# Optimization experiments

Measured on AMD Instinct MI355X. Metric: run time of the kernel, lower is better.

## Reference

```python
import jax, jax.numpy as jnp
import numpy as np

BN_EPS = 1e-5  # torch BatchNorm1d default


def _batchnorm(x, gamma, beta):
    # x: [B, N, H]. torch BatchNorm1d on 3D input normalizes per channel (dim 1 = N)
    # over batch and last dim, using biased variance (training mode).
    mean = jnp.mean(x, axis=(0, 2), keepdims=True)
    var = jnp.var(x, axis=(0, 2), keepdims=True)
    return gamma[None, :, None] * (x - mean) / jnp.sqrt(var + BN_EPS) + beta[None, :, None]


def setup_inputs() -> dict:
    key = jax.random.key(0)
    ks = jax.random.split(key, 8)
    B, N, D, Hd = 4, 256, 128, 256
    # symmetric Bernoulli(0.05) adjacency, zero diagonal
    raw = (jax.random.uniform(ks[0], (B, N, N)) < 0.05).astype(jnp.float32)
    A = jnp.maximum(raw, jnp.swapaxes(raw, 1, 2))
    A = A * (1.0 - jnp.eye(N, dtype=jnp.float32))
    X = jax.random.normal(ks[1], (B, N, D), dtype=jnp.float32)

    def lin(k, fi, fo):
        return (jax.random.normal(k, (fi, fo), dtype=jnp.float32) / np.sqrt(fi).astype(np.float32))

    W1 = lin(ks[2], D, Hd); b1 = jnp.zeros((Hd,), jnp.float32)
    g1 = jnp.ones((N,), jnp.float32); be1 = jnp.zeros((N,), jnp.float32)
    W2 = lin(ks[3], Hd, Hd); b2 = jnp.zeros((Hd,), jnp.float32)
    g2 = jnp.ones((N,), jnp.float32); be2 = jnp.zeros((N,), jnp.float32)
    W3 = lin(ks[4], D, Hd); b3 = jnp.zeros((Hd,), jnp.float32)
    W4 = lin(ks[5], Hd, D); b4 = jnp.zeros((D,), jnp.float32)
    eps = jnp.full((1,), 0.1, dtype=jnp.float32)  # reset_parameters: 0.1/sqrt(1)
    return dict(A=A, X=X, eps=eps, W1=W1, b1=b1, g1=g1, be1=be1,
                W2=W2, b2=b2, g2=g2, be2=be2, W3=W3, b3=b3, W4=W4, b4=b4)


def reference(A, X, eps, W1, b1, g1, be1, W2, b2, g2, be2, W3, b3, W4, b4):
    B, N, D = X.shape
    I = jnp.eye(N, dtype=A.dtype)
    # standard GIN-style propagation: ((1+eps)*I + A) @ X
    X_std = ((1.0 + eps[0]) * I[None, :, :] + A) @ X

    # triangle/pair aggregation. Original: for node i, for each neighbor pair
    # (j<k) with A[j,k] != 0, add mlp2(X[j]+X[k]).
    # Vectorized: X_pw[b,i] = sum_{j<k} A[b,i,j]*A[b,i,k]*A[b,j,k]*mlp2(X[b,j]+X[b,k])
    P = X[:, :, None, :] + X[:, None, :, :]                       # [B,N,N,D] pair sums
    Fp = jax.nn.relu(jax.nn.relu(P @ W3 + b3) @ W4 + b4)          # mlp2 (dropout p=0)
    triu = jnp.triu(jnp.ones((N, N), A.dtype), k=1)               # j<k only
    G = (A * triu)[..., None] * Fp                                # [B,N,N,D]
    X_pw = jnp.einsum('bij,bik,bjkd->bid', A, A, G)

    Xn = X_std + X_pw
    # mlp1: Linear -> Dropout(0) -> ReLU -> BN -> Linear -> Dropout(0) -> ReLU -> BN
    h = _batchnorm(jax.nn.relu(Xn @ W1 + b1), g1, be1)
    h = _batchnorm(jax.nn.relu(h @ W2 + b2), g2, be2)
    return h
```

## Files before the change

kernel.cpp:

```cpp
#include <hip/hip_runtime.h>
#include <hip/hip_bf16.h>
#include <stdint.h>

#define B 4
#define N 256
#define D 128
#define H 256
#define MAXE 4096
#define SLOTCAP 256

typedef __attribute__((ext_vector_type(8))) short bf16x8;
typedef __attribute__((ext_vector_type(4))) float f32x4;

__device__ __forceinline__ ushort f2b(float f) {
  __hip_bfloat16 h = __float2bfloat16(f);
  return *reinterpret_cast<ushort*>(&h);
}
__device__ __forceinline__ float b2f(ushort u) {
  return __uint_as_float(((unsigned)u) << 16);
}

#define SWZ(off, row) ((off) ^ (((row) & 7) << 4))

__global__ __launch_bounds__(64) void k_adj(
    const float* __restrict__ A, const float* __restrict__ W3,
    const float* __restrict__ W4,
    uint64_t* __restrict__ adjMask, unsigned* __restrict__ deg,
    uint8_t* __restrict__ nbr, unsigned* __restrict__ rowBase,
    unsigned* __restrict__ edgeCnt, unsigned* __restrict__ edges,
    ushort* __restrict__ W3T, ushort* __restrict__ W4T) {
  int bid = blockIdx.x, lane = threadIdx.x;
  if (bid >= B * N) {
    int idx = (bid - B * N) * 64 + lane;
    if (idx < D * H) {
      int h = idx >> 7, c = idx & 127;
      W3T[h * D + c] = f2b(W3[c * H + h]);
    } else {
      int i2 = idx - D * H;
      int d = i2 >> 8, hh = i2 & 255;
      W4T[d * H + hh] = f2b(W4[hh * D + d]);
    }
    return;
  }
  int row = bid;
  int b = row >> 8, j = row & 255;
  const float* Arow = A + (size_t)row * N;
  uint64_t m0 = __ballot(Arow[lane] != 0.0f);
  uint64_t m1 = __ballot(Arow[64 + lane] != 0.0f);
  uint64_t m2 = __ballot(Arow[128 + lane] != 0.0f);
  uint64_t m3 = __ballot(Arow[192 + lane] != 0.0f);
  if (lane == 0) {
    adjMask[row * 4 + 0] = m0; adjMask[row * 4 + 1] = m1;
    adjMask[row * 4 + 2] = m2; adjMask[row * 4 + 3] = m3;
  }
  int c0 = __popcll(m0), c1 = __popcll(m1), c2 = __popcll(m2), c3 = __popcll(m3);
  int total = min(c0 + c1 + c2 + c3, 64);
  if (lane == 0) deg[row] = (unsigned)total;
  uint64_t lt = (1ull << lane) - 1ull;
  uint8_t* nr = nbr + (size_t)row * 64;
  if ((m0 >> lane) & 1) { int s = __popcll(m0 & lt);              if (s < 64) nr[s] = (uint8_t)lane; }
  if ((m1 >> lane) & 1) { int s = c0 + __popcll(m1 & lt);         if (s < 64) nr[s] = (uint8_t)(64+lane); }
  if ((m2 >> lane) & 1) { int s = c0+c1 + __popcll(m2 & lt);      if (s < 64) nr[s] = (uint8_t)(128+lane); }
  if ((m3 >> lane) & 1) { int s = c0+c1+c2 + __popcll(m3 & lt);   if (s < 64) nr[s] = (uint8_t)(192+lane); }
  auto gtm = [&](int c) -> uint64_t {
    int lo = j - c * 64;
    if (lo < 0) return ~0ull;
    if (lo >= 63) return 0ull;
    return ~((2ull << lo) - 1ull);
  };
  uint64_t e0 = m0 & gtm(0), e1 = m1 & gtm(1), e2 = m2 & gtm(2), e3 = m3 & gtm(3);
  int t0c = __popcll(e0), t1c = __popcll(e1), t2c = __popcll(e2);
  int et = t0c + t1c + t2c + __popcll(e3);
  unsigned base = 0;
  if (lane == 0 && et) base = atomicAdd(&edgeCnt[b], (unsigned)et);
  base = (unsigned)__shfl((int)base, 0);
  if (lane == 0) rowBase[row] = base;
  unsigned* eb = edges + (size_t)b * MAXE;
  unsigned tag = ((unsigned)j << 8);
  if ((e0 >> lane) & 1) { unsigned s = base + __popcll(e0 & lt);               if (s < MAXE) eb[s] = tag | (unsigned)lane; }
  if ((e1 >> lane) & 1) { unsigned s = base + t0c + __popcll(e1 & lt);         if (s < MAXE) eb[s] = tag | (unsigned)(64+lane); }
  if ((e2 >> lane) & 1) { unsigned s = base + t0c+t1c + __popcll(e2 & lt);     if (s < MAXE) eb[s] = tag | (unsigned)(128+lane); }
  if ((e3 >> lane) & 1) { unsigned s = base + t0c+t1c+t2c + __popcll(e3 & lt); if (s < MAXE) eb[s] = tag | (unsigned)(192+lane); }
}

__global__ __launch_bounds__(256) void k_edge_mlp(
    const float* __restrict__ X, const unsigned* __restrict__ edges,
    const unsigned* __restrict__ edgeCnt,
    const ushort* __restrict__ W3T, const float* __restrict__ b3,
    const ushort* __restrict__ W4T, const float* __restrict__ b4,
    ushort* __restrict__ Fp) {
  __shared__ __align__(16) char smem[12288];
  __shared__ unsigned eLds[16];
  int blk = blockIdx.x;
  int b = blk >> 8, tile = blk & 255;
  unsigned cnt = min(edgeCnt[b], (unsigned)MAXE);
  int t0 = tile * 16;
  if ((unsigned)t0 >= cnt) return;
  int nE = min(16, (int)(cnt - (unsigned)t0));
  int tid = threadIdx.x;
  int w = tid >> 6, l = tid & 63, r = l & 15, g = l >> 4;
  const float* Xb = X + ((size_t)b * N) * D;

  if (tid < 16) eLds[tid] = (tid < nE) ? edges[(size_t)b * MAXE + t0 + tid] : 0u;
  __syncthreads();
  for (int idx = tid; idx < 16 * 64; idx += 256) {
    int e = idx >> 6, cp = idx & 63;
    unsigned ev = eLds[e];
    int j = (int)((ev >> 8) & 255u), k = (int)(ev & 255u);
    float2 xa = *(const float2*)(Xb + (size_t)j * D + cp * 2);
    float2 xb = *(const float2*)(Xb + (size_t)k * D + cp * 2);
    unsigned pk = (unsigned)f2b(xa.x + xb.x) | ((unsigned)f2b(xa.y + xb.y) << 16);
    *(unsigned*)(smem + e * 256 + SWZ(cp * 4, e)) = pk;
  }
  __syncthreads();
  {
    bf16x8 afr[4];
#pragma unroll
    for (int ks = 0; ks < 4; ++ks)
      afr[ks] = *(const bf16x8*)(smem + r * 256 + SWZ(ks * 64 + g * 16, r));
    f32x4 acc[4];
#pragma unroll
    for (int t4 = 0; t4 < 4; ++t4) acc[t4] = (f32x4){0.f, 0.f, 0.f, 0.f};
#pragma unroll
    for (int t4 = 0; t4 < 4; ++t4) {
      int h0 = w * 64 + t4 * 16 + r;
#pragma unroll
      for (int ks = 0; ks < 4; ++ks) {
        bf16x8 bfr = *(const bf16x8*)(W3T + (size_t)h0 * D + ks * 32 + g * 8);
        acc[t4] = __builtin_amdgcn_mfma_f32_16x16x32_bf16(afr[ks], bfr, acc[t4], 0, 0, 0);
      }
    }
#pragma unroll
    for (int t4 = 0; t4 < 4; ++t4) {
      int h0 = w * 64 + t4 * 16 + r;
      float bb = b3[h0];
#pragma unroll
      for (int jj = 0; jj < 4; ++jj) {
        int e = g * 4 + jj;
        float v = fmaxf(acc[t4][jj] + bb, 0.0f);
        *(ushort*)(smem + 4096 + e * 512 + SWZ(h0 * 2, e)) = f2b(v);
      }
    }
  }
  __syncthreads();
  {
    f32x4 acc2[2];
    acc2[0] = (f32x4){0.f, 0.f, 0.f, 0.f};
    acc2[1] = (f32x4){0.f, 0.f, 0.f, 0.f};
#pragma unroll
    for (int ks = 0; ks < 8; ++ks) {
      bf16x8 af = *(const bf16x8*)(smem + 4096 + r * 512 + SWZ(ks * 64 + g * 16, r));
#pragma unroll
      for (int t2 = 0; t2 < 2; ++t2) {
        int d0 = (w * 2 + t2) * 16 + r;
        bf16x8 bfr = *(const bf16x8*)(W4T + (size_t)d0 * H + ks * 32 + g * 8);
        acc2[t2] = __builtin_amdgcn_mfma_f32_16x16x32_bf16(af, bfr, acc2[t2], 0, 0, 0);
      }
    }
#pragma unroll
    for (int t2 = 0; t2 < 2; ++t2) {
      int d0 = (w * 2 + t2) * 16 + r;
      float bb = b4[d0];
#pragma unroll
      for (int jj = 0; jj < 4; ++jj) {
        int e = g * 4 + jj;
        if (e < nE) {
          float v = fmaxf(acc2[t2][jj] + bb, 0.0f);
          Fp[((size_t)b * MAXE + t0 + e) * D + d0] = f2b(v);
        }
      }
    }
  }
}

__global__ __launch_bounds__(512) void k_tail(
    const float* __restrict__ X, const float* __restrict__ eps,
    const ushort* __restrict__ Fp,
    const uint64_t* __restrict__ adjMask, const unsigned* __restrict__ rowBase,
    const unsigned* __restrict__ deg, const uint8_t* __restrict__ nbr,
    const float* __restrict__ W1, const float* __restrict__ b1,
    const float* __restrict__ g1, const float* __restrict__ be1,
    const float* __restrict__ W2, const float* __restrict__ b2,
    const float* __restrict__ g2, const float* __restrict__ be2,
    float* __restrict__ out) {
  __shared__ ushort slotsL[B][SLOTCAP];
  __shared__ uint8_t nbrL[B][64];
  __shared__ int    listLen[B], degL[B];
  __shared__ float  xr[B][D];
  __shared__ float  zr[B][H];
  __shared__ float  redS[8], redQ[8], bcast[2];
  int n = blockIdx.x, tid = threadIdx.x;
  int wv = tid >> 6, lane = tid & 63;

  if (wv < B) {
    int row = wv * N + n;
    int dg = (int)deg[row];
    if (lane == 0) degL[wv] = dg;
    uint64_t own0 = adjMask[(size_t)row * 4 + 0];
    uint64_t own1 = adjMask[(size_t)row * 4 + 1];
    uint64_t own2 = adjMask[(size_t)row * 4 + 2];
    uint64_t own3 = adjMask[(size_t)row * 4 + 3];
    uint64_t ej[4] = {0, 0, 0, 0}, cmv[4] = {0, 0, 0, 0};
    unsigned rbj = 0;
    int cnt = 0;
    if (lane < dg) {
      int j = (int)nbr[(size_t)row * 64 + lane];
      nbrL[wv][lane] = (uint8_t)j;
      const uint64_t* mj = adjMask + ((size_t)(wv * N + j)) * 4;
      rbj = rowBase[wv * N + j];
#pragma unroll
      for (int c = 0; c < 4; ++c) {
        int lo = j - c * 64;
        uint64_t gm = (lo < 0) ? ~0ull : (lo >= 63 ? 0ull : ~((2ull << lo) - 1ull));
        ej[c] = mj[c] & gm;
      }
      cmv[0] = ej[0] & own0; cmv[1] = ej[1] & own1;
      cmv[2] = ej[2] & own2; cmv[3] = ej[3] & own3;
      cnt = __popcll(cmv[0]) + __popcll(cmv[1]) + __popcll(cmv[2]) + __popcll(cmv[3]);
    }
    int off = cnt;
    for (int dd = 1; dd < 64; dd <<= 1) {
      int t = __shfl_up(off, dd);
      if (lane >= dd) off += t;
    }
    int excl = off - cnt;
    int total = __shfl(off, 63);
    if (lane == 63) listLen[wv] = min(total, SLOTCAP);
    if (lane < dg && cnt) {
      int idx = excl, pre = 0;
#pragma unroll
      for (int c = 0; c < 4; ++c) {
        uint64_t e = ej[c], m = cmv[c];
        while (m) {
          int lk = __builtin_ctzll(m);
          m &= m - 1;
          unsigned slot = rbj + (unsigned)(pre + __popcll(e & ((1ull << lk) - 1ull)));
          if (slot < (unsigned)MAXE && idx < SLOTCAP) slotsL[wv][idx++] = (ushort)slot;
        }
        pre += __popcll(e);
      }
    }
  }
  __syncthreads();

  {
    int p = tid >> 7, d = tid & 127;
    const float* Xb = X + ((size_t)p * N) * D;
    int dg = degL[p];
    float a0 = (1.0f + eps[0]) * Xb[(size_t)n * D + d];
    float a1 = 0.f, a2 = 0.f, a3 = 0.f;
    int s = 0;
    for (; s + 4 <= dg; s += 4) {
      a0 += Xb[(size_t)nbrL[p][s]     * D + d];
      a1 += Xb[(size_t)nbrL[p][s + 1] * D + d];
      a2 += Xb[(size_t)nbrL[p][s + 2] * D + d];
      a3 += Xb[(size_t)nbrL[p][s + 3] * D + d];
    }
    for (; s < dg; ++s) a0 += Xb[(size_t)nbrL[p][s] * D + d];
    int len = listLen[p];
    const ushort* FpB = Fp + (size_t)p * MAXE * D;
    s = 0;
    for (; s + 4 <= len; s += 4) {
      a0 += b2f(FpB[(size_t)slotsL[p][s]     * D + d]);
      a1 += b2f(FpB[(size_t)slotsL[p][s + 1] * D + d]);
      a2 += b2f(FpB[(size_t)slotsL[p][s + 2] * D + d]);
      a3 += b2f(FpB[(size_t)slotsL[p][s + 3] * D + d]);
    }
    for (; s < len; ++s) a0 += b2f(FpB[(size_t)slotsL[p][s] * D + d]);
    xr[p][d] = (a0 + a1) + (a2 + a3);
  }
  __syncthreads();

  float v0, v1;
  int half = tid >> 8, h = tid & 255;
  int r0 = half * 2, r1 = half * 2 + 1;
  {
    float a0 = b1[h], a1 = a0;
#pragma unroll 4
    for (int c = 0; c < D; c += 4) {
      float w0 = W1[(c + 0) * H + h];
      float w1 = W1[(c + 1) * H + h];
      float w2 = W1[(c + 2) * H + h];
      float w3 = W1[(c + 3) * H + h];
      float4 x0 = *(const float4*)&xr[r0][c];
      float4 x1 = *(const float4*)&xr[r1][c];
      a0 = fmaf(x0.x, w0, fmaf(x0.y, w1, fmaf(x0.z, w2, fmaf(x0.w, w3, a0))));
      a1 = fmaf(x1.x, w0, fmaf(x1.y, w1, fmaf(x1.z, w2, fmaf(x1.w, w3, a1))));
    }
    v0 = fmaxf(a0, 0.f); v1 = fmaxf(a1, 0.f);
  }
  {
    float s = v0 + v1, q = v0 * v0 + v1 * v1;
    for (int o = 32; o; o >>= 1) { s += __shfl_down(s, o); q += __shfl_down(q, o); }
    if (lane == 0) { redS[wv] = s; redQ[wv] = q; }
    __syncthreads();
    if (tid == 0) {
      float S = 0.f, Q = 0.f;
#pragma unroll
      for (int i = 0; i < 8; ++i) { S += redS[i]; Q += redQ[i]; }
      float mean = S * (1.0f / 1024.0f);
      float var = Q * (1.0f / 1024.0f) - mean * mean;
      float inv = rsqrtf(var + 1e-5f);
      float aa = g1[blockIdx.x] * inv;
      bcast[0] = aa;
      bcast[1] = be1[blockIdx.x] - aa * mean;
    }
    __syncthreads();
    float aa = bcast[0], cc = bcast[1];
    zr[r0][h] = fmaf(aa, v0, cc);
    zr[r1][h] = fmaf(aa, v1, cc);
  }
  __syncthreads();

  {
    float a0 = b2[h], a1 = a0;
#pragma unroll 4
    for (int c = 0; c < H; c += 4) {
      float w0 = W2[(c + 0) * H + h];
      float w1 = W2[(c + 1) * H + h];
      float w2 = W2[(c + 2) * H + h];
      float w3 = W2[(c + 3) * H + h];
      float4 z0 = *(const float4*)&zr[r0][c];
      float4 z1 = *(const float4*)&zr[r1][c];
      a0 = fmaf(z0.x, w0, fmaf(z0.y, w1, fmaf(z0.z, w2, fmaf(z0.w, w3, a0))));
      a1 = fmaf(z1.x, w0, fmaf(z1.y, w1, fmaf(z1.z, w2, fmaf(z1.w, w3, a1))));
    }
    v0 = fmaxf(a0, 0.f); v1 = fmaxf(a1, 0.f);
  }
  {
    float s = v0 + v1, q = v0 * v0 + v1 * v1;
    for (int o = 32; o; o >>= 1) { s += __shfl_down(s, o); q += __shfl_down(q, o); }
    if (lane == 0) { redS[wv] = s; redQ[wv] = q; }
    __syncthreads();
    if (tid == 0) {
      float S = 0.f, Q = 0.f;
#pragma unroll
      for (int i = 0; i < 8; ++i) { S += redS[i]; Q += redQ[i]; }
      float mean = S * (1.0f / 1024.0f);
      float var = Q * (1.0f / 1024.0f) - mean * mean;
      float inv = rsqrtf(var + 1e-5f);
      float aa = g2[blockIdx.x] * inv;
      bcast[0] = aa;
      bcast[1] = be2[blockIdx.x] - aa * mean;
    }
    __syncthreads();
    float aa = bcast[0], cc = bcast[1];
    out[((size_t)(r0 * N + blockIdx.x)) * H + h] = fmaf(aa, v0, cc);
    out[((size_t)(r1 * N + blockIdx.x)) * H + h] = fmaf(aa, v1, cc);
  }
}

extern "C" void kernel_launch(void* const* d_in, const int* in_sizes, int n_in,
                              void* d_out, int out_size, void* d_ws, size_t ws_size,
                              hipStream_t stream) {
  const float* A   = (const float*)d_in[0];
  const float* X   = (const float*)d_in[1];
  const float* eps = (const float*)d_in[2];
  const float* W1  = (const float*)d_in[3];
  const float* b1  = (const float*)d_in[4];
  const float* g1  = (const float*)d_in[5];
  const float* be1 = (const float*)d_in[6];
  const float* W2  = (const float*)d_in[7];
  const float* b2  = (const float*)d_in[8];
  const float* g2  = (const float*)d_in[9];
  const float* be2 = (const float*)d_in[10];
  const float* W3  = (const float*)d_in[11];
  const float* b3  = (const float*)d_in[12];
  const float* W4  = (const float*)d_in[13];
  const float* b4  = (const float*)d_in[14];
  float* out = (float*)d_out;

  char* ws = (char*)d_ws;
  auto take = [&](size_t bytes) { char* r = ws; ws += (bytes + 255) & ~(size_t)255; return r; };
  unsigned* edgeCnt = (unsigned*)take(256);
  uint64_t* adjMask = (uint64_t*)take((size_t)B * N * 4 * 8);
  unsigned* rowBase = (unsigned*)take((size_t)B * N * 4);
  unsigned* edges   = (unsigned*)take((size_t)B * MAXE * 4);
  unsigned* deg     = (unsigned*)take((size_t)B * N * 4);
  uint8_t*  nbr     = (uint8_t*)take((size_t)B * N * 64);
  ushort*   W3T     = (ushort*)take((size_t)D * H * 2);
  ushort*   W4T     = (ushort*)take((size_t)D * H * 2);
  ushort*   Fp      = (ushort*)take((size_t)B * MAXE * D * 2);

  hipMemsetAsync(edgeCnt, 0, 256, stream);

  k_adj<<<B * N + 1024, 64, 0, stream>>>(
      A, W3, W4, adjMask, deg, nbr, rowBase, edgeCnt, edges, W3T, W4T);
  k_edge_mlp<<<B * 256, 256, 0, stream>>>(
      X, edges, edgeCnt, W3T, b3, W4T, b4, Fp);
  k_tail<<<N, 512, 0, stream>>>(
      X, eps, Fp, adjMask, rowBase, deg, nbr, W1, b1, g1, be1, W2, b2, g2, be2, out);
}
```

Measured before the change: 146.7 us.

## Move GIN neighbor aggregation from tail kernel into adjacency kernel

The (1+eps)X + A@X neighbor gather now runs in the adjacency kernel, which grows to 128 threads per row block and writes an intermediate Xn buffer. The tail kernel reads Xn instead of gathering neighbor rows itself. The gather is spread over 1024 blocks instead of 256, taking it off the serialized tail kernel. The cost is an extra global write and read of Xn and a heavier first kernel.

```diff
diff --git a/kernel.cpp b/kernel.cpp
--- a/kernel.cpp
+++ b/kernel.cpp
@@ -22,16 +22,18 @@
 
 #define SWZ(off, row) ((off) ^ (((row) & 7) << 4))
 
-__global__ __launch_bounds__(64) void k_adj(
-    const float* __restrict__ A, const float* __restrict__ W3,
+__global__ __launch_bounds__(128) void k_adj_xstd(
+    const float* __restrict__ A, const float* __restrict__ X,
+    const float* __restrict__ eps, const float* __restrict__ W3,
     const float* __restrict__ W4,
     uint64_t* __restrict__ adjMask, unsigned* __restrict__ deg,
     uint8_t* __restrict__ nbr, unsigned* __restrict__ rowBase,
     unsigned* __restrict__ edgeCnt, unsigned* __restrict__ edges,
-    ushort* __restrict__ W3T, ushort* __restrict__ W4T) {
-  int bid = blockIdx.x, lane = threadIdx.x;
+    ushort* __restrict__ W3T, ushort* __restrict__ W4T,
+    float* __restrict__ Xn) {
+  int bid = blockIdx.x, tid = threadIdx.x;
   if (bid >= B * N) {
-    int idx = (bid - B * N) * 64 + lane;
+    int idx = (bid - B * N) * 128 + tid;
     if (idx < D * H) {
       int h = idx >> 7, c = idx & 127;
       W3T[h * D + c] = f2b(W3[c * H + h]);
@@ -42,45 +44,65 @@
     }
     return;
   }
+  __shared__ uint8_t nbrL[64];
+  __shared__ int degL;
   int row = bid;
   int b = row >> 8, j = row & 255;
-  const float* Arow = A + (size_t)row * N;
-  uint64_t m0 = __ballot(Arow[lane] != 0.0f);
-  uint64_t m1 = __ballot(Arow[64 + lane] != 0.0f);
-  uint64_t m2 = __ballot(Arow[128 + lane] != 0.0f);
-  uint64_t m3 = __ballot(Arow[192 + lane] != 0.0f);
-  if (lane == 0) {
-    adjMask[row * 4 + 0] = m0; adjMask[row * 4 + 1] = m1;
-    adjMask[row * 4 + 2] = m2; adjMask[row * 4 + 3] = m3;
-  }
-  int c0 = __popcll(m0), c1 = __popcll(m1), c2 = __popcll(m2), c3 = __popcll(m3);
-  int total = min(c0 + c1 + c2 + c3, 64);
-  if (lane == 0) deg[row] = (unsigned)total;
-  uint64_t lt = (1ull << lane) - 1ull;
-  uint8_t* nr = nbr + (size_t)row * 64;
-  if ((m0 >> lane) & 1) { int s = __popcll(m0 & lt);              if (s < 64) nr[s] = (uint8_t)lane; }
-  if ((m1 >> lane) & 1) { int s = c0 + __popcll(m1 & lt);         if (s < 64) nr[s] = (uint8_t)(64+lane); }
-  if ((m2 >> lane) & 1) { int s = c0+c1 + __popcll(m2 & lt);      if (s < 64) nr[s] = (uint8_t)(128+lane); }
-  if ((m3 >> lane) & 1) { int s = c0+c1+c2 + __popcll(m3 & lt);   if (s < 64) nr[s] = (uint8_t)(192+lane); }
-  auto gtm = [&](int c) -> uint64_t {
-    int lo = j - c * 64;
-    if (lo < 0) return ~0ull;
-    if (lo >= 63) return 0ull;
-    return ~((2ull << lo) - 1ull);
-  };
-  uint64_t e0 = m0 & gtm(0), e1 = m1 & gtm(1), e2 = m2 & gtm(2), e3 = m3 & gtm(3);
-  int t0c = __popcll(e0), t1c = __popcll(e1), t2c = __popcll(e2);
-  int et = t0c + t1c + t2c + __popcll(e3);
-  unsigned base = 0;
-  if (lane == 0 && et) base = atomicAdd(&edgeCnt[b], (unsigned)et);
-  base = (unsigned)__shfl((int)base, 0);
-  if (lane == 0) rowBase[row] = base;
-  unsigned* eb = edges + (size_t)b * MAXE;
-  unsigned tag = ((unsigned)j << 8);
-  if ((e0 >> lane) & 1) { unsigned s = base + __popcll(e0 & lt);               if (s < MAXE) eb[s] = tag | (unsigned)lane; }
-  if ((e1 >> lane) & 1) { unsigned s = base + t0c + __popcll(e1 & lt);         if (s < MAXE) eb[s] = tag | (unsigned)(64+lane); }
-  if ((e2 >> lane) & 1) { unsigned s = base + t0c+t1c + __popcll(e2 & lt);     if (s < MAXE) eb[s] = tag | (unsigned)(128+lane); }
-  if ((e3 >> lane) & 1) { unsigned s = base + t0c+t1c+t2c + __popcll(e3 & lt); if (s < MAXE) eb[s] = tag | (unsigned)(192+lane); }
+  if (tid < 64) {
+    int lane = tid;
+    const float* Arow = A + (size_t)row * N;
+    uint64_t m0 = __ballot(Arow[lane] != 0.0f);
+    uint64_t m1 = __ballot(Arow[64 + lane] != 0.0f);
+    uint64_t m2 = __ballot(Arow[128 + lane] != 0.0f);
+    uint64_t m3 = __ballot(Arow[192 + lane] != 0.0f);
+    if (lane == 0) {
+      adjMask[row * 4 + 0] = m0; adjMask[row * 4 + 1] = m1;
+      adjMask[row * 4 + 2] = m2; adjMask[row * 4 + 3] = m3;
+    }
+    int c0 = __popcll(m0), c1 = __popcll(m1), c2 = __popcll(m2), c3 = __popcll(m3);
+    int total = min(c0 + c1 + c2 + c3, 64);
+    if (lane == 0) { deg[row] = (unsigned)total; degL = total; }
+    uint64_t lt = (1ull << lane) - 1ull;
+    uint8_t* nr = nbr + (size_t)row * 64;
+    if ((m0 >> lane) & 1) { int s = __popcll(m0 & lt);              if (s < 64) { nr[s] = (uint8_t)lane;       nbrL[s] = (uint8_t)lane; } }
+    if ((m1 >> lane) & 1) { int s = c0 + __popcll(m1 & lt);         if (s < 64) { nr[s] = (uint8_t)(64+lane);  nbrL[s] = (uint8_t)(64+lane); } }
+    if ((m2 >> lane) & 1) { int s = c0+c1 + __popcll(m2 & lt);      if (s < 64) { nr[s] = (uint8_t)(128+lane); nbrL[s] = (uint8_t)(128+lane); } }
+    if ((m3 >> lane) & 1) { int s = c0+c1+c2 + __popcll(m3 & lt);   if (s < 64) { nr[s] = (uint8_t)(192+lane); nbrL[s] = (uint8_t)(192+lane); } }
+    auto gtm = [&](int c) -> uint64_t {
+      int lo = j - c * 64;
+      if (lo < 0) return ~0ull;
+      if (lo >= 63) return 0ull;
+      return ~((2ull << lo) - 1ull);
+    };
+    uint64_t e0 = m0 & gtm(0), e1 = m1 & gtm(1), e2 = m2 & gtm(2), e3 = m3 & gtm(3);
+    int t0c = __popcll(e0), t1c = __popcll(e1), t2c = __popcll(e2);
+    int et = t0c + t1c + t2c + __popcll(e3);
+    unsigned base = 0;
+    if (lane == 0 && et) base = atomicAdd(&edgeCnt[b], (unsigned)et);
+    base = (unsigned)__shfl((int)base, 0);
+    if (lane == 0) rowBase[row] = base;
+    unsigned* eb = edges + (size_t)b * MAXE;
+    unsigned tag = ((unsigned)j << 8);
+    if ((e0 >> lane) & 1) { unsigned s = base + __popcll(e0 & lt);               if (s < MAXE) eb[s] = tag | (unsigned)lane; }
+    if ((e1 >> lane) & 1) { unsigned s = base + t0c + __popcll(e1 & lt);         if (s < MAXE) eb[s] = tag | (unsigned)(64+lane); }
+    if ((e2 >> lane) & 1) { unsigned s = base + t0c+t1c + __popcll(e2 & lt);     if (s < MAXE) eb[s] = tag | (unsigned)(128+lane); }
+    if ((e3 >> lane) & 1) { unsigned s = base + t0c+t1c+t2c + __popcll(e3 & lt); if (s < MAXE) eb[s] = tag | (unsigned)(192+lane); }
+  }
+  __syncthreads();
+  int d = tid;
+  int dg = degL;
+  const float* Xb = X + ((size_t)b * N) * D;
+  float a0 = (1.0f + eps[0]) * Xb[(size_t)j * D + d];
+  float a1 = 0.f, a2 = 0.f, a3 = 0.f;
+  int s = 0;
+  for (; s + 4 <= dg; s += 4) {
+    a0 += Xb[(size_t)nbrL[s]     * D + d];
+    a1 += Xb[(size_t)nbrL[s + 1] * D + d];
+    a2 += Xb[(size_t)nbrL[s + 2] * D + d];
+    a3 += Xb[(size_t)nbrL[s + 3] * D + d];
+  }
+  for (; s < dg; ++s) a0 += Xb[(size_t)nbrL[s] * D + d];
+  Xn[(size_t)row * D + d] = (a0 + a1) + (a2 + a3);
 }
 
 __global__ __launch_bounds__(256) void k_edge_mlp(
@@ -174,8 +196,7 @@
 }
 
 __global__ __launch_bounds__(512) void k_tail(
-    const float* __restrict__ X, const float* __restrict__ eps,
-    const ushort* __restrict__ Fp,
+    const float* __restrict__ Xn, const ushort* __restrict__ Fp,
     const uint64_t* __restrict__ adjMask, const unsigned* __restrict__ rowBase,
     const unsigned* __restrict__ deg, const uint8_t* __restrict__ nbr,
     const float* __restrict__ W1, const float* __restrict__ b1,
@@ -184,8 +205,7 @@
     const float* __restrict__ g2, const float* __restrict__ be2,
     float* __restrict__ out) {
   __shared__ ushort slotsL[B][SLOTCAP];
-  __shared__ uint8_t nbrL[B][64];
-  __shared__ int    listLen[B], degL[B];
+  __shared__ int    listLen[B];
   __shared__ float  xr[B][D];
   __shared__ float  zr[B][H];
   __shared__ float  redS[8], redQ[8], bcast[2];
@@ -195,7 +215,6 @@
   if (wv < B) {
     int row = wv * N + n;
     int dg = (int)deg[row];
-    if (lane == 0) degL[wv] = dg;
     uint64_t own0 = adjMask[(size_t)row * 4 + 0];
     uint64_t own1 = adjMask[(size_t)row * 4 + 1];
     uint64_t own2 = adjMask[(size_t)row * 4 + 2];
@@ -205,7 +224,6 @@
     int cnt = 0;
     if (lane < dg) {
       int j = (int)nbr[(size_t)row * 64 + lane];
-      nbrL[wv][lane] = (uint8_t)j;
       const uint64_t* mj = adjMask + ((size_t)(wv * N + j)) * 4;
       rbj = rowBase[wv * N + j];
 #pragma unroll
@@ -245,21 +263,11 @@
 
   {
     int p = tid >> 7, d = tid & 127;
-    const float* Xb = X + ((size_t)p * N) * D;
-    int dg = degL[p];
-    float a0 = (1.0f + eps[0]) * Xb[(size_t)n * D + d];
+    int len = listLen[p];
+    const ushort* FpB = Fp + (size_t)p * MAXE * D;
+    float a0 = Xn[((size_t)(p * N + n)) * D + d];
     float a1 = 0.f, a2 = 0.f, a3 = 0.f;
     int s = 0;
-    for (; s + 4 <= dg; s += 4) {
-      a0 += Xb[(size_t)nbrL[p][s]     * D + d];
-      a1 += Xb[(size_t)nbrL[p][s + 1] * D + d];
-      a2 += Xb[(size_t)nbrL[p][s + 2] * D + d];
-      a3 += Xb[(size_t)nbrL[p][s + 3] * D + d];
-    }
-    for (; s < dg; ++s) a0 += Xb[(size_t)nbrL[p][s] * D + d];
-    int len = listLen[p];
-    const ushort* FpB = Fp + (size_t)p * MAXE * D;
-    s = 0;
     for (; s + 4 <= len; s += 4) {
       a0 += b2f(FpB[(size_t)slotsL[p][s]     * D + d]);
       a1 += b2f(FpB[(size_t)slotsL[p][s + 1] * D + d]);
@@ -380,14 +388,15 @@
   uint8_t*  nbr     = (uint8_t*)take((size_t)B * N * 64);
   ushort*   W3T     = (ushort*)take((size_t)D * H * 2);
   ushort*   W4T     = (ushort*)take((size_t)D * H * 2);
+  float*    Xn      = (float*)take((size_t)B * N * D * 4);
   ushort*   Fp      = (ushort*)take((size_t)B * MAXE * D * 2);
 
   hipMemsetAsync(edgeCnt, 0, 256, stream);
 
-  k_adj<<<B * N + 1024, 64, 0, stream>>>(
-      A, W3, W4, adjMask, deg, nbr, rowBase, edgeCnt, edges, W3T, W4T);
+  k_adj_xstd<<<B * N + 512, 128, 0, stream>>>(
+      A, X, eps, W3, W4, adjMask, deg, nbr, rowBase, edgeCnt, edges, W3T, W4T, Xn);
   k_edge_mlp<<<B * 256, 256, 0, stream>>>(
       X, edges, edgeCnt, W3T, b3, W4T, b4, Fp);
   k_tail<<<N, 512, 0, stream>>>(
-      X, eps, Fp, adjMask, rowBase, deg, nbr, W1, b1, g1, be1, W2, b2, g2, be2, out);
-}
+      Xn, Fp, adjMask, rowBase, deg, nbr, W1, b1, g1, be1, W2, b2, g2, be2, out);
+}
```

Result: faster. 135.2 us (-7.8%).
